# Performance work log

Measured on AMD Instinct MI355X. Metric: run time of the kernel, lower is better.

Reference implementation:

```python
import jax, jax.numpy as jnp
import numpy as np

M = 8192   # output rows
N = 8192   # input dim
K = 8192   # non_zero_rows (inner dim after dropping empty B rows)
NNZ_A = 256  # nonzeros per row of A (m x k)
NNZ_B = 256  # nonzeros per row of B (k x n)
BATCH = 32


def setup_inputs() -> dict:
    key = jax.random.key(0)
    k1, k2, k3, k4, k5 = jax.random.split(key, 5)
    x = jax.random.normal(k1, (N, BATCH), dtype=jnp.float32)
    a_idx = jax.random.randint(k2, (M, NNZ_A), 0, K, dtype=jnp.int32)
    a_vals = jax.random.normal(k3, (M, NNZ_A), dtype=jnp.float32) * 0.05
    b_idx = jax.random.randint(k4, (K, NNZ_B), 0, N, dtype=jnp.int32)
    b_vals = jax.random.normal(k5, (K, NNZ_B), dtype=jnp.float32) * 0.05
    return {"x": x, "a_idx": a_idx, "a_vals": a_vals, "b_idx": b_idx, "b_vals": b_vals}


def reference(x, a_idx, a_vals, b_idx, b_vals):
    # Double-sparse matvec: y = A @ (B @ x), sparse matrices in ELL form
    # (row-wise column indices + values, equivalent math to the CSR kernel).
    # B @ x: gather x rows per nonzero of B, contract over nnz axis.
    bx = jnp.einsum('kj,kjb->kb', b_vals, x[b_idx])        # [K, BATCH]
    # A @ bx: gather bx rows per nonzero of A.
    y = jnp.einsum('mj,mjb->mb', a_vals, bx[a_idx])        # [M, BATCH]
    # Match torch output layout: (1, batch, m)
    return y.T[None]
```

## Files before the change

kernel.cpp:

```cpp
#include <hip/hip_runtime.h>


#define NNZ    256
#define BATCH  32
#define ROWS   8192

typedef int      vi4 __attribute__((ext_vector_type(4)));
typedef float    vf4 __attribute__((ext_vector_type(4)));
typedef _Float16 vh4 __attribute__((ext_vector_type(4)));
typedef _Float16 vh8 __attribute__((ext_vector_type(8)));

__global__ __launch_bounds__(256) void cvt_f32_f16(
    const float* __restrict__ src, _Float16* __restrict__ dst)
{
    const int i = blockIdx.x * 256 + threadIdx.x;
    const vf4 v = *(const vf4*)(src + i * 4);
    vh4 h;
    h.x = (_Float16)v.x; h.y = (_Float16)v.y;
    h.z = (_Float16)v.z; h.w = (_Float16)v.w;
    *(vh4*)(dst + i * 4) = h;
}

template <bool OUT16>
__global__ __launch_bounds__(256) void ell_spmv_h(
    const int*      __restrict__ idx,
    const float*    __restrict__ vals,
    const _Float16* __restrict__ src,
    _Float16*       __restrict__ dst16,
    float*          __restrict__ dst32)
{
    __shared__ float tile[4][BATCH];

    const int wave = threadIdx.x >> 6;
    const int lane = threadIdx.x & 63;
    const int r    = blockIdx.x * 4 + wave;
    const int s    = lane & 3;
    const int q    = lane >> 2;

    const vi4* i4 = (const vi4*)(idx  + r * NNZ) + q * 4;
    const vf4* v4 = (const vf4*)(vals + r * NNZ) + q * 4;
    const int  soff = s * 8;

    vi4 iv[4]; vf4 vv[4];
    #pragma unroll
    for (int t = 0; t < 4; ++t) iv[t] = __builtin_nontemporal_load(i4 + t);
    #pragma unroll
    for (int t = 0; t < 4; ++t) vv[t] = __builtin_nontemporal_load(v4 + t);

    vh8 acc = {0, 0, 0, 0, 0, 0, 0, 0};

    #pragma unroll
    for (int t = 0; t < 4; ++t) {
        const _Float16 h0 = (_Float16)vv[t].x, h1 = (_Float16)vv[t].y;
        const _Float16 h2 = (_Float16)vv[t].z, h3 = (_Float16)vv[t].w;
        {
            const vh8 xv = *(const vh8*)(src + iv[t].x * BATCH + soff);
            const vh8 b = {h0, h0, h0, h0, h0, h0, h0, h0};
            acc += b * xv;
        }
        {
            const vh8 xv = *(const vh8*)(src + iv[t].y * BATCH + soff);
            const vh8 b = {h1, h1, h1, h1, h1, h1, h1, h1};
            acc += b * xv;
        }
        {
            const vh8 xv = *(const vh8*)(src + iv[t].z * BATCH + soff);
            const vh8 b = {h2, h2, h2, h2, h2, h2, h2, h2};
            acc += b * xv;
        }
        {
            const vh8 xv = *(const vh8*)(src + iv[t].w * BATCH + soff);
            const vh8 b = {h3, h3, h3, h3, h3, h3, h3, h3};
            acc += b * xv;
        }
    }

    float a32[8];
    #pragma unroll
    for (int j = 0; j < 8; ++j) a32[j] = (float)acc[j];

    #pragma unroll
    for (int d = 4; d < 64; d <<= 1) {
        #pragma unroll
        for (int j = 0; j < 8; ++j) a32[j] += __shfl_xor(a32[j], d);
    }

    if (OUT16) {
        if (q == 0) {
            vh8 h;
            #pragma unroll
            for (int j = 0; j < 8; ++j) h[j] = (_Float16)a32[j];
            *(vh8*)(dst16 + r * BATCH + soff) = h;
        }
    } else {
        if (q == 0) {
            #pragma unroll
            for (int j = 0; j < 8; ++j) tile[wave][soff + j] = a32[j];
        }
        __syncthreads();
        const int t = threadIdx.x;
        if (t < 4 * BATCH) {
            const int b  = t >> 2;
            const int rr = t & 3;
            __builtin_nontemporal_store(tile[rr][b],
                                        dst32 + b * ROWS + blockIdx.x * 4 + rr);
        }
    }
}

extern "C" void kernel_launch(void* const* d_in, const int* in_sizes, int n_in,
                              void* d_out, int out_size, void* d_ws, size_t ws_size,
                              hipStream_t stream) {
    const float* x      = (const float*)d_in[0];
    const int*   a_idx  = (const int*)  d_in[1];
    const float* a_vals = (const float*)d_in[2];
    const int*   b_idx  = (const int*)  d_in[3];
    const float* b_vals = (const float*)d_in[4];
    float*       out    = (float*)d_out;

    _Float16* bx16 = (_Float16*)d_ws;
    _Float16* x16  = (_Float16*)d_ws + (size_t)ROWS * BATCH;

    dim3 block(256);

    cvt_f32_f16<<<dim3(ROWS * BATCH / 4 / 256), block, 0, stream>>>(x, x16);
    ell_spmv_h<true ><<<dim3(ROWS / 4), block, 0, stream>>>(
        b_idx, b_vals, x16, bx16, nullptr);
    ell_spmv_h<false><<<dim3(ROWS / 4), block, 0, stream>>>(
        a_idx, a_vals, bx16, nullptr, out);
}
```

Measured before the change: 111.2 us.

## Stage dense operand segments in LDS and gather from shared memory

Each block of 512 threads now handles 32 rows. The fp16 dense operand is streamed through a 128KB LDS buffer in four 2048-row segments using global_load_lds. Every nonzero is processed in all four passes, with its weight zeroed when its index falls outside the current segment, so the random global gathers become LDS reads at the cost of four times the FMA and LDS traffic. The output transpose also gains padded tiles and float2 stores. Risks are low occupancy from the 128KB of LDS and the redundant masked work.

```diff
diff --git a/kernel.cpp b/kernel.cpp
--- a/kernel.cpp
+++ b/kernel.cpp
@@ -1,14 +1,21 @@
 #include <hip/hip_runtime.h>
 
 
-#define NNZ    256
-#define BATCH  32
-#define ROWS   8192
+#define NNZ     256
+#define BATCH   32
+#define ROWS    8192
+#define SEGR    2048
+#define NSEG    4
+#define RPB     32
+#define THREADS 512
 
 typedef int      vi4 __attribute__((ext_vector_type(4)));
 typedef float    vf4 __attribute__((ext_vector_type(4)));
+typedef _Float16 vh2 __attribute__((ext_vector_type(2)));
 typedef _Float16 vh4 __attribute__((ext_vector_type(4)));
 typedef _Float16 vh8 __attribute__((ext_vector_type(8)));
+
+union V8 { vh8 h8; vh2 h2[4]; unsigned u[4]; };
 
 __global__ __launch_bounds__(256) void cvt_f32_f16(
     const float* __restrict__ src, _Float16* __restrict__ dst)
@@ -21,96 +28,146 @@
     *(vh4*)(dst + i * 4) = h;
 }
 
+static __device__ __forceinline__ unsigned hpack(float f)
+{
+    const unsigned short u = __builtin_bit_cast(unsigned short, (_Float16)f);
+    return ((unsigned)u << 16) | (unsigned)u;
+}
+
+#define PROC(K, BB)                                                           \
+    do {                                                                      \
+        const int k_ = (K);                                                   \
+        V8 xv_;                                                               \
+        xv_.h8 = *(const vh8*)(lb + ((((unsigned)k_ & 2047u) << 6) + soffb)); \
+        const unsigned sel_ = ((k_ >> 11) == p) ? (BB) : 0u;                  \
+        const vh2 b2_ = __builtin_bit_cast(vh2, sel_);                        \
+        acc[t].h2[0] += b2_ * xv_.h2[0];                                      \
+        acc[t].h2[1] += b2_ * xv_.h2[1];                                      \
+        acc[t].h2[2] += b2_ * xv_.h2[2];                                      \
+        acc[t].h2[3] += b2_ * xv_.h2[3];                                      \
+    } while (0)
+
 template <bool OUT16>
-__global__ __launch_bounds__(256) void ell_spmv_h(
+__global__ __launch_bounds__(THREADS, 2) void ell_spmv_lds(
     const int*      __restrict__ idx,
     const float*    __restrict__ vals,
     const _Float16* __restrict__ src,
     _Float16*       __restrict__ dst16,
     float*          __restrict__ dst32)
 {
-    __shared__ float tile[4][BATCH];
+    __shared__ __attribute__((aligned(16))) _Float16 lds[SEGR * BATCH];
 
-    const int wave = threadIdx.x >> 6;
-    const int lane = threadIdx.x & 63;
-    const int r    = blockIdx.x * 4 + wave;
-    const int s    = lane & 3;
-    const int q    = lane >> 2;
+    const int tid   = threadIdx.x;
+    const int wave  = tid >> 6;
+    const int lane  = tid & 63;
+    const int s     = lane & 3;
+    const int q     = lane >> 2;
+    const int soffb = s * 16;
+    const int rbase = blockIdx.x * RPB;
 
-    const vi4* i4 = (const vi4*)(idx  + r * NNZ) + q * 4;
-    const vf4* v4 = (const vf4*)(vals + r * NNZ) + q * 4;
-    const int  soff = s * 8;
+    vi4      iv[4][4];
+    unsigned hh[4][16];
+    #pragma unroll
+    for (int t = 0; t < 4; ++t) {
+        const int r = rbase + wave * 4 + t;
+        const vi4* i4 = (const vi4*)(idx  + (size_t)r * NNZ) + q * 4;
+        const vf4* v4 = (const vf4*)(vals + (size_t)r * NNZ) + q * 4;
+        vf4 vv[4];
+        #pragma unroll
+        for (int u = 0; u < 4; ++u) iv[t][u] = __builtin_nontemporal_load(i4 + u);
+        #pragma unroll
+        for (int u = 0; u < 4; ++u) vv[u]    = __builtin_nontemporal_load(v4 + u);
+        #pragma unroll
+        for (int u = 0; u < 4; ++u) {
+            hh[t][4*u+0] = hpack(vv[u].x);
+            hh[t][4*u+1] = hpack(vv[u].y);
+            hh[t][4*u+2] = hpack(vv[u].z);
+            hh[t][4*u+3] = hpack(vv[u].w);
+        }
+    }
 
-    vi4 iv[4]; vf4 vv[4];
+    V8 acc[4];
     #pragma unroll
-    for (int t = 0; t < 4; ++t) iv[t] = __builtin_nontemporal_load(i4 + t);
-    #pragma unroll
-    for (int t = 0; t < 4; ++t) vv[t] = __builtin_nontemporal_load(v4 + t);
+    for (int t = 0; t < 4; ++t) {
+        acc[t].u[0] = 0; acc[t].u[1] = 0; acc[t].u[2] = 0; acc[t].u[3] = 0;
+    }
 
-    vh8 acc = {0, 0, 0, 0, 0, 0, 0, 0};
+    const char* lb = (const char*)lds;
+
+    #pragma unroll 1
+    for (int p = 0; p < NSEG; ++p) {
+        __syncthreads();
+        const char* gseg = (const char*)(src + (size_t)p * SEGR * BATCH);
+        #pragma unroll
+        for (int tch = 0; tch < 16; ++tch) {
+            const int off = tch * 8192 + tid * 16;
+            __builtin_amdgcn_global_load_lds(
+                (const __attribute__((address_space(1))) unsigned int*)(gseg + off),
+                (__attribute__((address_space(3))) unsigned int*)((char*)lds + off),
+                16, 0, 0);
+        }
+        __syncthreads();
+
+        #pragma unroll
+        for (int t = 0; t < 4; ++t) {
+            #pragma unroll
+            for (int u = 0; u < 4; ++u) {
+                PROC(iv[t][u].x, hh[t][4*u+0]);
+                PROC(iv[t][u].y, hh[t][4*u+1]);
+                PROC(iv[t][u].z, hh[t][4*u+2]);
+                PROC(iv[t][u].w, hh[t][4*u+3]);
+            }
+        }
+    }
+
+    float* tile = (float*)lds;
+    if (!OUT16) __syncthreads();
 
     #pragma unroll
     for (int t = 0; t < 4; ++t) {
-        const _Float16 h0 = (_Float16)vv[t].x, h1 = (_Float16)vv[t].y;
-        const _Float16 h2 = (_Float16)vv[t].z, h3 = (_Float16)vv[t].w;
-        {
-            const vh8 xv = *(const vh8*)(src + iv[t].x * BATCH + soff);
-            const vh8 b = {h0, h0, h0, h0, h0, h0, h0, h0};
-            acc += b * xv;
+        float a32[8];
+        #pragma unroll
+        for (int j = 0; j < 8; ++j) a32[j] = (float)acc[t].h8[j];
+        #pragma unroll
+        for (int d = 4; d < 64; d <<= 1) {
+            #pragma unroll
+            for (int j = 0; j < 8; ++j) a32[j] += __shfl_xor(a32[j], d);
         }
-        {
-            const vh8 xv = *(const vh8*)(src + iv[t].y * BATCH + soff);
-            const vh8 b = {h1, h1, h1, h1, h1, h1, h1, h1};
-            acc += b * xv;
-        }
-        {
-            const vh8 xv = *(const vh8*)(src + iv[t].z * BATCH + soff);
-            const vh8 b = {h2, h2, h2, h2, h2, h2, h2, h2};
-            acc += b * xv;
-        }
-        {
-            const vh8 xv = *(const vh8*)(src + iv[t].w * BATCH + soff);
-            const vh8 b = {h3, h3, h3, h3, h3, h3, h3, h3};
-            acc += b * xv;
+        if (OUT16) {
+            if (q == 0) {
+                const int r = rbase + wave * 4 + t;
+                vh8 h;
+                #pragma unroll
+                for (int j = 0; j < 8; ++j) h[j] = (_Float16)a32[j];
+                *(vh8*)(dst16 + (size_t)r * BATCH + s * 8) = h;
+            }
+        } else {
+            if (q == 0) {
+                const int rl = wave * 4 + t;
+                #pragma unroll
+                for (int j = 0; j < 8; ++j) tile[rl * 33 + s * 8 + j] = a32[j];
+            }
         }
     }
 
-    float a32[8];
-    #pragma unroll
-    for (int j = 0; j < 8; ++j) a32[j] = (float)acc[j];
-
-    #pragma unroll
-    for (int d = 4; d < 64; d <<= 1) {
-        #pragma unroll
-        for (int j = 0; j < 8; ++j) a32[j] += __shfl_xor(a32[j], d);
-    }
-
-    if (OUT16) {
-        if (q == 0) {
-            vh8 h;
-            #pragma unroll
-            for (int j = 0; j < 8; ++j) h[j] = (_Float16)a32[j];
-            *(vh8*)(dst16 + r * BATCH + soff) = h;
-        }
-    } else {
-        if (q == 0) {
-            #pragma unroll
-            for (int j = 0; j < 8; ++j) tile[wave][soff + j] = a32[j];
-        }
+    if (!OUT16) {
         __syncthreads();
-        const int t = threadIdx.x;
-        if (t < 4 * BATCH) {
-            const int b  = t >> 2;
-            const int rr = t & 3;
-            __builtin_nontemporal_store(tile[rr][b],
-                                        dst32 + b * ROWS + blockIdx.x * 4 + rr);
-        }
+        const int e  = tid * 2;
+        const int b  = e >> 5;
+        const int rr = e & 31;
+        float2 v2;
+        v2.x = tile[rr * 33 + b];
+        v2.y = tile[(rr + 1) * 33 + b];
+        *(float2*)(dst32 + (size_t)b * ROWS + rbase + rr) = v2;
     }
 }
+
+#undef PROC
 
 extern "C" void kernel_launch(void* const* d_in, const int* in_sizes, int n_in,
                               void* d_out, int out_size, void* d_ws, size_t ws_size,
                               hipStream_t stream) {
+    (void)in_sizes; (void)n_in; (void)out_size; (void)ws_size;
     const float* x      = (const float*)d_in[0];
     const int*   a_idx  = (const int*)  d_in[1];
     const float* a_vals = (const float*)d_in[2];
@@ -121,11 +178,9 @@
     _Float16* bx16 = (_Float16*)d_ws;
     _Float16* x16  = (_Float16*)d_ws + (size_t)ROWS * BATCH;
 
-    dim3 block(256);
-
-    cvt_f32_f16<<<dim3(ROWS * BATCH / 4 / 256), block, 0, stream>>>(x, x16);
-    ell_spmv_h<true ><<<dim3(ROWS / 4), block, 0, stream>>>(
+    cvt_f32_f16<<<dim3(ROWS * BATCH / 4 / 256), dim3(256), 0, stream>>>(x, x16);
+    ell_spmv_lds<true ><<<dim3(ROWS / RPB), dim3(THREADS), 0, stream>>>(
         b_idx, b_vals, x16, bx16, nullptr);
-    ell_spmv_h<false><<<dim3(ROWS / 4), block, 0, stream>>>(
+    ell_spmv_lds<false><<<dim3(ROWS / RPB), dim3(THREADS), 0, stream>>>(
         a_idx, a_vals, bx16, nullptr, out);
 }
```

Result: slower. 127.1 us (+14.3%).
